# Performance work log

Measured on AMD Instinct MI355X. Metric: run time of the kernel, lower is better.

Reference implementation:

```python
import jax, jax.numpy as jnp
import numpy as np

W_GRID, H_GRID = 5, 5
N_NODES = W_GRID * H_GRID  # 25
N_NEI = 8
N_CLS = 10
BN_EPS = 1e-5


def _neighbors(i, w, h):
    """Replicates Brain.neighbors ordering exactly; pads missing slots with -1
    (the torch code pads with p1 == zeros at the END of the list)."""
    size = w * h
    n = []
    if i - w >= 0:
        n.append(i - w)
    if i % w != 0:
        n.append(i - 1)
    if (i + 1) % w != 0:
        n.append(i + 1)
    if i + w < size:
        n.append(i + w)
    if i - w - 1 >= 0 and i % w != 0:
        n.append(i - w - 1)
    if i - w + 1 >= 0 and (i + 1) % w != 0:
        n.append(i - w + 1)
    if i + w - 1 < size and i % w != 0:
        n.append(i + w - 1)
    if i + w + 1 < size and (i + 1) % w != 0:
        n.append(i + w + 1)
    while len(n) < N_NEI:
        n.append(-1)
    return n

NEI = np.array([_neighbors(i, W_GRID, H_GRID) for i in range(N_NODES)], dtype=np.int32)  # [25, 8]
NEI_CLIP = np.maximum(NEI, 0)
NEI_MASK = (NEI >= 0)


def conv_bn_relu(x, W, b, g, be, m, v):
    # Conv2d(k=3, s=1, p=1) + eval-mode BatchNorm2d + ReLU, NCHW layout
    y = jax.lax.conv_general_dilated(
        x, W, window_strides=(1, 1), padding=[(1, 1), (1, 1)],
        dimension_numbers=("NCHW", "OIHW", "NCHW"))
    y = y + b[None, :, None, None]
    scale = g / jnp.sqrt(v + BN_EPS)
    y = (y - m[None, :, None, None]) * scale[None, :, None, None] + be[None, :, None, None]
    return jax.nn.relu(y)


def maxpool3s2p1(x):
    # MaxPool2d(kernel=3, stride=2, padding=1)
    return jax.lax.reduce_window(
        x, -jnp.inf, jax.lax.max,
        window_dimensions=(1, 1, 3, 3), window_strides=(1, 1, 2, 2),
        padding=[(0, 0), (0, 0), (1, 1), (1, 1)])


def per_node_mlp(inp, Wa, ba, Wb, bb):
    # inp: [25, B, 336]; distinct Linear(336,600)-Tanh-Linear(600,10)-Softmax per node
    h = jnp.tanh(jnp.einsum("nbi,nih->nbh", inp, Wa) + ba[:, None, :])
    logits = jnp.einsum("nbh,nhc->nbc", h, Wb) + bb[:, None, :]
    return jax.nn.softmax(logits, axis=-1)  # [25, B, 10]


def setup_inputs() -> dict:
    key = jax.random.key(0)
    ks = iter(jax.random.split(key, 64))
    B, C = 8192, 3
    d = {"x": jax.random.normal(next(ks), (B, C, 20, 20), jnp.float32)}
    chans = [(C, 64), (64, 128), (128, 256), (256, 256)]
    for li, (ci, co) in enumerate(chans, start=1):
        d[f"W{li}"] = jax.random.normal(next(ks), (co, ci, 3, 3), jnp.float32) * 0.05
        d[f"b{li}"] = jax.random.normal(next(ks), (co,), jnp.float32) * 0.05
        d[f"g{li}"] = jax.random.uniform(next(ks), (co,), jnp.float32, 0.5, 1.5)
        d[f"be{li}"] = jax.random.normal(next(ks), (co,), jnp.float32) * 0.1
        d[f"m{li}"] = jax.random.normal(next(ks), (co,), jnp.float32) * 0.1
        d[f"v{li}"] = jax.random.uniform(next(ks), (co,), jnp.float32, 0.5, 1.5)
    d["Wa"] = jax.random.normal(next(ks), (N_NODES, 336, 600), jnp.float32) * 0.05
    d["ba"] = jax.random.normal(next(ks), (N_NODES, 600), jnp.float32) * 0.05
    d["Wb"] = jax.random.normal(next(ks), (N_NODES, 600, N_CLS), jnp.float32) * 0.05
    d["bb"] = jax.random.normal(next(ks), (N_NODES, N_CLS), jnp.float32) * 0.05
    return d


def reference(x, W1, b1, g1, be1, m1, v1, W2, b2, g2, be2, m2, v2,
              W3, b3, g3, be3, m3, v3, W4, b4, g4, be4, m4, v4,
              Wa, ba, Wb, bb):
    c = conv_bn_relu(x, W1, b1, g1, be1, m1, v1)
    c = maxpool3s2p1(c)                      # [B, 64, 10, 10]
    c = conv_bn_relu(c, W2, b2, g2, be2, m2, v2)
    c = maxpool3s2p1(c)                      # [B, 128, 5, 5]
    c = conv_bn_relu(c, W3, b3, g3, be3, m3, v3)
    c = conv_bn_relu(c, W4, b4, g4, be4, m4, v4)  # [B, 256, 5, 5]
    B = x.shape[0]
    feats = c.reshape(B, 256, N_NODES).transpose(2, 0, 1)  # [25, B, 256]
    # Stage 1: neighbor slots are all zeros (p1..p8 = zeros)
    zeros80 = jnp.zeros((N_NODES, B, N_NEI * N_CLS), x.dtype)
    preds = per_node_mlp(jnp.concatenate([zeros80, feats], axis=-1), Wa, ba, Wb, bb)  # [25, B, 10]
    # Stage 2: gather up to 8 neighbor predictions (ordered), pad missing with zeros
    nb = preds[jnp.asarray(NEI_CLIP)]                          # [25, 8, B, 10]
    nb = jnp.where(jnp.asarray(NEI_MASK)[:, :, None, None], nb, 0.0)
    nb = nb.transpose(0, 2, 1, 3).reshape(N_NODES, B, N_NEI * N_CLS)  # [25, B, 80]
    second = per_node_mlp(jnp.concatenate([nb, feats], axis=-1), Wa, ba, Wb, bb)  # [25, B, 10]
    mean_predictions = second.mean(axis=0)  # [B, 10]
    return mean_predictions, second
```

## Files before the change

### kernel.cpp

```cpp
#include <hip/hip_runtime.h>

typedef unsigned short u16;
typedef unsigned int u32;

typedef __attribute__((ext_vector_type(8))) __bf16 bf16x8;
typedef __attribute__((ext_vector_type(4))) float f32x4;

__device__ __forceinline__ float bf2f(u16 u) {
    u32 t = ((u32)u) << 16;
    float f;
    __builtin_memcpy(&f, &t, 4);
    return f;
}
__device__ __forceinline__ u16 f2bf(float f) {
    u32 u;
    __builtin_memcpy(&u, &f, 4);
    u32 r = (u + 0x7fffu + ((u >> 16) & 1u)) >> 16;
    return (u16)r;
}
__device__ __forceinline__ float tanh_fast(float x) {
    float xc = fminf(fmaxf(x, -15.f), 15.f);
    float e = __expf(2.f * xc);
    return (e - 1.f) * __builtin_amdgcn_rcpf(e + 1.f);
}

__device__ __forceinline__ void gld16(const u16* g, u16* l) {
    __builtin_amdgcn_global_load_lds(
        (const __attribute__((address_space(1))) u32*)(uintptr_t)g,
        (__attribute__((address_space(3))) u32*)(u32)(uintptr_t)l,
        16, 0, 0);
}


template <int EPI, int NT>
__global__ __launch_bounds__(256, 3) void gemm_bt(
    const u16* __restrict__ A, const u16* __restrict__ W, u16* __restrict__ O,
    const float* __restrict__ epiA, const float* __restrict__ epiB,
    int Kin, int N, int T, int Himg, int Wimg,
    int ldA, int ldW, int ldO,
    long long Az, long long Wz, long long Oz, int epiZ,
    int Bc, int bshift)
{
    constexpr int NJ = NT / 32;
    __shared__ __align__(16) u16 lsA[2][128 * 32];
    __shared__ __align__(16) u16 lsW[2][NT * 32];

    const int tid = threadIdx.x;
    const int z = blockIdx.z;
    A += (long long)z * Az;
    W += (long long)z * Wz;
    O += (long long)z * Oz;
    epiB += (long long)z * epiZ;

    const int m0 = blockIdx.x * 128;
    const int n0 = blockIdx.y * NT;
    const int s = m0 >> bshift;
    const int b0 = m0 & (Bc - 1);
    const int hh0 = s / Wimg, ww0 = s % Wimg;

    const int wave = tid >> 6;
    const int lane = tid & 63;
    const int mbase = (wave >> 1) * 64;
    const int nbase = (wave & 1) * (NT / 2);
    const int ln = lane & 15, qd = lane >> 4;

    const int srow = lane >> 2;
    const int sc = (((lane & 3) - ((srow >> 1) & 3)) & 3) * 8;
    const int csel = ((qd + (ln >> 1)) & 3) * 8;

    const int rowA = wave * 32 + srow;
    const int rowW = (NT == 128) ? (wave * 32 + srow) : (wave * 16 + srow);
    const int offA0 = rowA * ldA + sc;
    const int offA1 = offA0 + 16 * ldA;
    const int offW0 = rowW * ldW + sc;
    const int offW1 = offW0 + 16 * ldW;
    u16* const lA0 = &lsA[0][0] + wave * 1024;
    u16* const lW0 = (NT == 128) ? (&lsW[0][0] + wave * 1024) : (&lsW[0][0] + wave * 512);
    constexpr int LPAR_A = 128 * 32;
    constexpr int LPAR_W = NT * 32;

    auto tapvalid = [&](int t) -> bool {
        if (T != 9) return true;
        const int hh = hh0 + t / 3 - 1, ww = ww0 + t % 3 - 1;
        return hh >= 0 && hh < Himg && ww >= 0 && ww < Wimg;
    };
    auto tapA = [&](int t) -> const u16* {
        int sp = s;
        if (T == 9) sp = (hh0 + t / 3 - 1) * Wimg + (ww0 + t % 3 - 1);
        return A + (long long)(sp * Bc + b0) * ldA;
    };

    int t0 = 0;
    while (!tapvalid(t0)) ++t0;
    int nvalid = 0;
    for (int t = 0; t < T; ++t) nvalid += tapvalid(t) ? 1 : 0;
    const int KS = Kin >> 5;
    const int S = nvalid * KS;

    const u16* Ab = tapA(t0);
    const u16* Wb = W + ((long long)t0 * N + n0) * ldW;

    gld16(Ab + offA0, lA0);
    gld16(Ab + offA1, lA0 + 512);
    gld16(Wb + offW0, lW0);
    if (NT == 128) gld16(Wb + offW1, lW0 + 512);

    int ntap = t0, nkk = 0;

    f32x4 acc[4][NJ];
#pragma unroll
    for (int i = 0; i < 4; ++i)
#pragma unroll
        for (int j = 0; j < NJ; ++j)
            acc[i][j] = (f32x4){0.f, 0.f, 0.f, 0.f};

    for (int st = 0; st < S; ++st) {
        __syncthreads();
        if (st + 1 < S) {
            nkk += 32;
            if (nkk == Kin) {
                nkk = 0;
                do { ++ntap; } while (!tapvalid(ntap));
                Ab = tapA(ntap);
                Wb = W + ((long long)ntap * N + n0) * ldW;
            }
            const int pp = (st + 1) & 1;
            gld16(Ab + offA0 + nkk, lA0 + pp * LPAR_A);
            gld16(Ab + offA1 + nkk, lA0 + pp * LPAR_A + 512);
            gld16(Wb + offW0 + nkk, lW0 + pp * LPAR_W);
            if (NT == 128) gld16(Wb + offW1 + nkk, lW0 + pp * LPAR_W + 512);
        }
        const int cp = st & 1;
        bf16x8 af[4], bfr[NJ];
#pragma unroll
        for (int f = 0; f < 4; ++f)
            af[f] = *(const bf16x8*)&lsA[cp][(mbase + f * 16 + ln) * 32 + csel];
#pragma unroll
        for (int f = 0; f < NJ; ++f)
            bfr[f] = *(const bf16x8*)&lsW[cp][(nbase + f * 16 + ln) * 32 + csel];
#pragma unroll
        for (int i = 0; i < 4; ++i)
#pragma unroll
            for (int j = 0; j < NJ; ++j)
                acc[i][j] = __builtin_amdgcn_mfma_f32_16x16x32_bf16(
                    af[i], bfr[j], acc[i][j], 0, 0, 0);
    }

#pragma unroll
    for (int j = 0; j < NJ; ++j) {
        const int n = n0 + nbase + j * 16 + ln;
        const float sh = epiB[n];
        float sc2 = 1.f;
        if (EPI == 0) sc2 = epiA[n];
#pragma unroll
        for (int i = 0; i < 4; ++i) {
            const int mrow = mbase + i * 16 + qd * 4;
#pragma unroll
            for (int rr = 0; rr < 4; ++rr) {
                float v = acc[i][j][rr];
                if (EPI == 0) v = fmaxf(v * sc2 + sh, 0.f);
                else          v = tanh_fast(v + sh);
                O[(long long)(m0 + mrow + rr) * ldO + n] = f2bf(v);
            }
        }
    }
}

template <int STAGE>
__global__ __launch_bounds__(256, 2) void mlp_head(
    const u16* __restrict__ A, const u16* __restrict__ W,
    const float* __restrict__ bap, const u16* __restrict__ Wbp,
    const float* __restrict__ bbp,
    u16* __restrict__ preds, float* __restrict__ dout,
    int Kin, int Bc, int gbase)
{
    __shared__ __align__(16) u16 lsA[2][128 * 32];
    __shared__ __align__(16) u16 lsW[2][128 * 32];
    __shared__ __align__(16) u16 lsH[128 * 132];

    const int tid = threadIdx.x;
    const int z = blockIdx.z;
    A += (long long)z * Bc * Kin;
    W += (long long)z * 640 * 352;
    const float* bz = bap + z * 640;

    const int m0 = blockIdx.x * 128;
    const int wave = tid >> 6;
    const int lane = tid & 63;
    const int mbase = (wave >> 1) * 64;
    const int nbase = (wave & 1) * 64;
    const int ln = lane & 15, qd = lane >> 4;
    const int srow = lane >> 2;
    const int sc = (((lane & 3) - ((srow >> 1) & 3)) & 3) * 8;
    const int csel = ((qd + (ln >> 1)) & 3) * 8;

    const int rowS = wave * 32 + srow;
    const int offA0 = rowS * Kin + sc;
    const int offA1 = offA0 + 16 * Kin;
    const int offW0 = rowS * 352 + sc;
    const int offW1 = offW0 + 16 * 352;
    u16* const lA0 = &lsA[0][0] + wave * 1024;
    u16* const lW0 = &lsW[0][0] + wave * 1024;

    const int KS = Kin >> 5;
    const int Stot = 5 * KS;

    const u16* Ab = A + (long long)m0 * Kin;
    const u16* Wb = W;
    int pnt = 0, pnkk = 0;

    gld16(Ab + offA0, lA0);
    gld16(Ab + offA1, lA0 + 512);
    gld16(Wb + offW0, lW0);
    gld16(Wb + offW1, lW0 + 512);

    f32x4 acc[4][4];
#pragma unroll
    for (int i = 0; i < 4; ++i)
#pragma unroll
        for (int j = 0; j < 4; ++j)
            acc[i][j] = (f32x4){0.f, 0.f, 0.f, 0.f};
    f32x4 acc_lg[2];
    acc_lg[0] = (f32x4){0.f, 0.f, 0.f, 0.f};
    acc_lg[1] = (f32x4){0.f, 0.f, 0.f, 0.f};

    int g = 0;
    for (int nt = 0; nt < 5; ++nt) {
        for (int st = 0; st < KS; ++st, ++g) {
            __syncthreads();
            if (g + 1 < Stot) {
                pnkk += 32;
                if (pnkk == Kin) {
                    pnkk = 0;
                    ++pnt;
                    Wb = W + (long long)pnt * 128 * 352;
                }
                const int pp = (g + 1) & 1;
                gld16(Ab + offA0 + pnkk, lA0 + pp * (128 * 32));
                gld16(Ab + offA1 + pnkk, lA0 + pp * (128 * 32) + 512);
                gld16(Wb + offW0 + pnkk, lW0 + pp * (128 * 32));
                gld16(Wb + offW1 + pnkk, lW0 + pp * (128 * 32) + 512);
            }
            const int cp = g & 1;
            bf16x8 af[4], bfr[4];
#pragma unroll
            for (int f = 0; f < 4; ++f)
                af[f] = *(const bf16x8*)&lsA[cp][(mbase + f * 16 + ln) * 32 + csel];
#pragma unroll
            for (int f = 0; f < 4; ++f)
                bfr[f] = *(const bf16x8*)&lsW[cp][(nbase + f * 16 + ln) * 32 + csel];
#pragma unroll
            for (int i = 0; i < 4; ++i)
#pragma unroll
                for (int j = 0; j < 4; ++j)
                    acc[i][j] = __builtin_amdgcn_mfma_f32_16x16x32_bf16(
                        af[i], bfr[j], acc[i][j], 0, 0, 0);
        }

#pragma unroll
        for (int j = 0; j < 4; ++j) {
            const int hc = nbase + j * 16 + ln;
            const float sh = bz[nt * 128 + hc];
#pragma unroll
            for (int i = 0; i < 4; ++i) {
                const int br = mbase + i * 16 + qd * 4;
#pragma unroll
                for (int rr = 0; rr < 4; ++rr)
                    lsH[(br + rr) * 132 + hc] = f2bf(tanh_fast(acc[i][j][rr] + sh));
                acc[i][j] = (f32x4){0.f, 0.f, 0.f, 0.f};
            }
        }
        bf16x8 bfrg[4];
#pragma unroll
        for (int ks = 0; ks < 4; ++ks)
            bfrg[ks] = *(const bf16x8*)&Wbp[((long long)z * 16 + ln) * 640 +
                                            nt * 128 + ks * 32 + qd * 8];
        __syncthreads();

#pragma unroll
        for (int ks = 0; ks < 4; ++ks) {
#pragma unroll
            for (int i = 0; i < 2; ++i) {
                const int base = (wave * 32 + i * 16 + ln) * 132 + ks * 32 + qd * 8;
                const uint2 u0 = *(const uint2*)&lsH[base];
                const uint2 u1 = *(const uint2*)&lsH[base + 4];
                u32 w4[4] = {u0.x, u0.y, u1.x, u1.y};
                bf16x8 a8;
                __builtin_memcpy(&a8, w4, 16);
                acc_lg[i] = __builtin_amdgcn_mfma_f32_16x16x32_bf16(
                    a8, bfrg[ks], acc_lg[i], 0, 0, 0);
            }
        }
    }

    const float bias = bbp[z * 16 + ln];
#pragma unroll
    for (int i = 0; i < 2; ++i) {
#pragma unroll
        for (int rr = 0; rr < 4; ++rr) {
            const float v = acc_lg[i][rr] + bias;
            float mx = v;
#pragma unroll
            for (int mk = 1; mk < 16; mk <<= 1)
                mx = fmaxf(mx, __shfl_xor(mx, mk));
            const float e = __expf(v - mx);
            float ssum = e;
#pragma unroll
            for (int mk = 1; mk < 16; mk <<= 1)
                ssum += __shfl_xor(ssum, mk);
            const float p = e / ssum;
            const int row = m0 + wave * 32 + i * 16 + qd * 4 + rr;
            if (ln < 10) {
                if (STAGE == 1)
                    preds[((long long)z * Bc + row) * 10 + ln] = f2bf(p);
                else
                    dout[81920 + ((long long)z * 8192 + gbase + row) * 10 + ln] = p;
            }
        }
    }
}

__global__ __launch_bounds__(256) void conv1pool(
    const u16* __restrict__ xcol, const u16* __restrict__ W1t, u16* __restrict__ p1,
    const float* __restrict__ epiA, const float* __restrict__ epiB, int Bc)
{
    const int tid = threadIdx.x;
    const int wave = tid >> 6;
    const int lane = tid & 63;
    const int ln = lane & 15, qd = lane >> 4;

    const int b0 = blockIdx.x * 128;
    const int so = blockIdx.y;
    const int ho = so / 10, wo = so % 10;

    const int mbase = (wave >> 1) * 64;
    const int nbase = (wave & 1) * 32;

    bf16x8 bfr[2];
#pragma unroll
    for (int j = 0; j < 2; ++j)
        bfr[j] = *(const bf16x8*)&W1t[(nbase + j * 16 + ln) * 32 + qd * 8];

    float sc2[2], sh[2];
#pragma unroll
    for (int j = 0; j < 2; ++j) {
        const int n = nbase + j * 16 + ln;
        sc2[j] = epiA[n];
        sh[j] = epiB[n];
    }

    f32x4 best[4][2];
#pragma unroll
    for (int i = 0; i < 4; ++i)
#pragma unroll
        for (int j = 0; j < 2; ++j)
            best[i][j] = (f32x4){0.f, 0.f, 0.f, 0.f};

#pragma unroll
    for (int st = 0; st < 9; ++st) {
        int hh = 2 * ho - 1 + st / 3;
        int ww = 2 * wo - 1 + st % 3;
        hh = hh < 0 ? 0 : (hh > 19 ? 19 : hh);
        ww = ww < 0 ? 0 : (ww > 19 ? 19 : ww);
        const u16* Ab = xcol + (long long)((hh * 20 + ww) * Bc + b0) * 32;

        bf16x8 af[4];
#pragma unroll
        for (int f = 0; f < 4; ++f)
            af[f] = *(const bf16x8*)&Ab[(mbase + f * 16 + ln) * 32 + qd * 8];

#pragma unroll
        for (int i = 0; i < 4; ++i)
#pragma unroll
            for (int j = 0; j < 2; ++j) {
                f32x4 acc = (f32x4){0.f, 0.f, 0.f, 0.f};
                acc = __builtin_amdgcn_mfma_f32_16x16x32_bf16(af[i], bfr[j], acc, 0, 0, 0);
#pragma unroll
                for (int rr = 0; rr < 4; ++rr) {
                    const float v = fmaxf(acc[rr] * sc2[j] + sh[j], 0.f);
                    best[i][j][rr] = fmaxf(best[i][j][rr], v);
                }
            }
    }

#pragma unroll
    for (int j = 0; j < 2; ++j) {
        const int n = nbase + j * 16 + ln;
#pragma unroll
        for (int i = 0; i < 4; ++i) {
            const int mrow = mbase + i * 16 + qd * 4;
#pragma unroll
            for (int rr = 0; rr < 4; ++rr)
                p1[(long long)(so * Bc + b0 + mrow + rr) * 64 + n] = f2bf(best[i][j][rr]);
        }
    }
}

__global__ __launch_bounds__(256) void transpose_x(
    const float* __restrict__ x, u16* __restrict__ xt, int Bc, int bshift)
{
    const int t = blockIdx.x * 256 + threadIdx.x;
    if (t >= 400 * Bc) return;
    const int s = t >> bshift;
    const int b = t & (Bc - 1);
    const u32 c0 = f2bf(x[((long long)b * 3 + 0) * 400 + s]);
    const u32 c1 = f2bf(x[((long long)b * 3 + 1) * 400 + s]);
    const u32 c2 = f2bf(x[((long long)b * 3 + 2) * 400 + s]);
    uint2 st;
    st.x = c0 | (c1 << 16);
    st.y = c2;
    *(uint2*)(xt + ((long long)s * Bc + b) * 4) = st;
}

__global__ __launch_bounds__(256) void im2col1(
    const u16* __restrict__ xt, u16* __restrict__ xcol, int Bc, int bshift)
{
    const int t = blockIdx.x * 256 + threadIdx.x;
    if (t >= 400 * Bc) return;
    const int s = t >> bshift;
    const int b = t & (Bc - 1);
    const int hh = s / 20, ww = s % 20;

    u32 p0, q0, p1, q1, p2, q2, p3, q3, p4, q4, p5, q5, p6, q6, p7, q7, p8, q8;
#define LOADTAP(T, P, Q)                                                      \
    {                                                                         \
        const int ih = hh + (T) / 3 - 1, iw = ww + (T) % 3 - 1;               \
        P = 0u; Q = 0u;                                                       \
        if (ih >= 0 && ih < 20 && iw >= 0 && iw < 20) {                       \
            const uint2 v = *(const uint2*)(xt +                              \
                ((long long)(ih * 20 + iw) * Bc + b) * 4);                    \
            P = v.x; Q = v.y;                                                 \
        }                                                                     \
    }
    LOADTAP(0, p0, q0) LOADTAP(1, p1, q1) LOADTAP(2, p2, q2)
    LOADTAP(3, p3, q3) LOADTAP(4, p4, q4) LOADTAP(5, p5, q5)
    LOADTAP(6, p6, q6) LOADTAP(7, p7, q7) LOADTAP(8, p8, q8)
#undef LOADTAP

    u16* o = xcol + (long long)t * 32;
    uint4 w;
    w.x = p0;                w.y = q0 | (p1 << 16);
    w.z = (p1 >> 16) | (q1 << 16);
    w.w = p2;
    *(uint4*)(o + 0) = w;
    w.x = q2 | (p3 << 16);   w.y = (p3 >> 16) | (q3 << 16);
    w.z = p4;                w.w = q4 | (p5 << 16);
    *(uint4*)(o + 8) = w;
    w.x = (p5 >> 16) | (q5 << 16);
    w.y = p6;                w.z = q6 | (p7 << 16);
    w.w = (p7 >> 16) | (q7 << 16);
    *(uint4*)(o + 16) = w;
    w.x = p8;                w.y = q8;
    w.z = 0u;                w.w = 0u;
    *(uint4*)(o + 24) = w;
}

template <int CH>
__global__ __launch_bounds__(256) void pool_k(
    const u16* __restrict__ src, u16* __restrict__ dst, int Bc, int Hi, int Ho)
{
    constexpr int G = CH / 8;
    const int t = blockIdx.x * 256 + threadIdx.x;
    const int cc = t & (G - 1);
    const int b = t / G;
    if (b >= Bc) return;
    const int so = blockIdx.y;
    const int ho = so / Ho, wo = so % Ho;
    float best[8];
#pragma unroll
    for (int e = 0; e < 8; ++e) best[e] = 0.f;
    for (int ph = 0; ph < 3; ++ph) {
        const int hh = 2 * ho - 1 + ph;
        if (hh < 0 || hh >= Hi) continue;
        for (int pw = 0; pw < 3; ++pw) {
            const int ww = 2 * wo - 1 + pw;
            if (ww < 0 || ww >= Hi) continue;
            const uint4 u = *(const uint4*)(src + ((long long)(hh * Hi + ww) * Bc + b) * CH + cc * 8);
            const u32 uw[4] = {u.x, u.y, u.z, u.w};
#pragma unroll
            for (int e = 0; e < 4; ++e) {
                best[2 * e]     = fmaxf(best[2 * e],     bf2f((u16)(uw[e] & 0xffff)));
                best[2 * e + 1] = fmaxf(best[2 * e + 1], bf2f((u16)(uw[e] >> 16)));
            }
        }
    }
    u32 pk[4];
#pragma unroll
    for (int e = 0; e < 4; ++e)
        pk[e] = (u32)f2bf(best[2 * e]) | (((u32)f2bf(best[2 * e + 1])) << 16);
    uint4 st;
    st.x = pk[0]; st.y = pk[1]; st.z = pk[2]; st.w = pk[3];
    *(uint4*)(dst + ((long long)so * Bc + b) * CH + cc * 8) = st;
}

__device__ __forceinline__ void neighbors5x5(int i, int* nb) {
    const int w = 5, size = 25;
    int cnt = 0;
    if (i - w >= 0) nb[cnt++] = i - w;
    if (i % w != 0) nb[cnt++] = i - 1;
    if ((i + 1) % w != 0) nb[cnt++] = i + 1;
    if (i + w < size) nb[cnt++] = i + w;
    if (i - w - 1 >= 0 && i % w != 0) nb[cnt++] = i - w - 1;
    if (i - w + 1 >= 0 && (i + 1) % w != 0) nb[cnt++] = i - w + 1;
    if (i + w - 1 < size && i % w != 0) nb[cnt++] = i + w - 1;
    if (i + w + 1 < size && (i + 1) % w != 0) nb[cnt++] = i + w + 1;
    for (; cnt < 8; ++cnt) nb[cnt] = -1;
}

__global__ __launch_bounds__(256) void gather_nb(
    const u16* __restrict__ preds, const u16* __restrict__ feats, u16* __restrict__ A2,
    int Bc, int bshift)
{
    const int g = blockIdx.x * 256 + threadIdx.x;
    if (g >= 25 * Bc) return;
    const int n = g >> bshift;
    const int b = g & (Bc - 1);
    int nb[8];
    neighbors5x5(n, nb);
    u16* dst = A2 + (long long)g * 352;
#pragma unroll
    for (int j = 0; j < 8; ++j) {
        u32* d32 = (u32*)(dst + j * 10);
        if (nb[j] >= 0) {
            const u32* s32 = (const u32*)(preds + ((long long)nb[j] * Bc + b) * 10);
#pragma unroll
            for (int q = 0; q < 5; ++q) d32[q] = s32[q];
        } else {
#pragma unroll
            for (int q = 0; q < 5; ++q) d32[q] = 0u;
        }
    }
    const uint4* fs = (const uint4*)(feats + (long long)g * 256);
    uint4* fd = (uint4*)(dst + 80);
#pragma unroll
    for (int q = 0; q < 32; ++q) fd[q] = fs[q];
    uint4 z;
    z.x = 0u; z.y = 0u; z.z = 0u; z.w = 0u;
    *(uint4*)(dst + 336) = z;
    *(uint4*)(dst + 344) = z;
}

__global__ __launch_bounds__(256) void mean_k(float* __restrict__ dout)
{
    const int t = blockIdx.x * 256 + threadIdx.x;
    float s = 0.f;
#pragma unroll
    for (int n = 0; n < 25; ++n) s += dout[81920 + n * 81920 + t];
    dout[t] = s * 0.04f;
}

__global__ void prep_bn_all(
    const float* b1, const float* g1, const float* be1, const float* m1, const float* v1,
    const float* b2, const float* g2, const float* be2, const float* m2, const float* v2,
    const float* b3, const float* g3, const float* be3, const float* m3, const float* v3,
    const float* b4, const float* g4, const float* be4, const float* m4, const float* v4,
    float* bnA, float* bnB)
{
    const int t = blockIdx.x * 256 + threadIdx.x;
    if (t >= 704) return;
    const float *bp, *gp, *bep, *mp, *vp;
    int idx;
    if (t < 64)       { bp=b1; gp=g1; bep=be1; mp=m1; vp=v1; idx=t; }
    else if (t < 192) { bp=b2; gp=g2; bep=be2; mp=m2; vp=v2; idx=t-64; }
    else if (t < 448) { bp=b3; gp=g3; bep=be3; mp=m3; vp=v3; idx=t-192; }
    else              { bp=b4; gp=g4; bep=be4; mp=m4; vp=v4; idx=t-448; }
    const float A = gp[idx] * rsqrtf(vp[idx] + 1e-5f);
    bnA[t] = A;
    bnB[t] = (bp[idx] - mp[idx]) * A + bep[idx];
}

__global__ void prep_w1col(const float* __restrict__ W1, u16* __restrict__ W1t)
{
    const int t = blockIdx.x * 256 + threadIdx.x;
    if (t >= 64 * 32) return;
    const int n = t >> 5, k = t & 31;
    u16 v = 0;
    if (k < 27) {
        const int tap = k / 3, ci = k % 3;
        v = f2bf(W1[n * 27 + ci * 9 + tap]);
    }
    W1t[t] = v;
}

__global__ void prep_convw(const float* __restrict__ W, u16* __restrict__ Wt, int Co, int Ci)
{
    const int t = blockIdx.x * 256 + threadIdx.x;
    const int tot = 9 * Co * Ci;
    if (t >= tot) return;
    const int sh = t / (Co * Ci);
    const int rem = t % (Co * Ci);
    const int co = rem / Ci, ci = rem % Ci;
    Wt[t] = f2bf(W[(long long)(co * Ci + ci) * 9 + sh]);
}

__global__ void prep_wat(const float* __restrict__ Wa, u16* __restrict__ Wat)
{
    const int t = blockIdx.x * 256 + threadIdx.x;
    if (t >= 25 * 640 * 352) return;
    const int n = t / (640 * 352);
    const int rem = t % (640 * 352);
    const int hcol = rem / 352;
    const int k = rem % 352;
    float v = 0.f;
    if (hcol < 600 && k < 336) v = Wa[((long long)n * 336 + k) * 600 + hcol];
    Wat[t] = f2bf(v);
}

__global__ void prep_ba(const float* __restrict__ ba, float* __restrict__ bap)
{
    const int t = blockIdx.x * 256 + threadIdx.x;
    if (t >= 25 * 640) return;
    const int n = t / 640, hcol = t % 640;
    bap[t] = (hcol < 600) ? ba[n * 600 + hcol] : 0.f;
}

__global__ void prep_wbt(const float* __restrict__ Wb, const float* __restrict__ bb,
                         u16* __restrict__ Wbp, float* __restrict__ bbp)
{
    const int t = blockIdx.x * 256 + threadIdx.x;
    if (t < 25 * 16 * 640) {
        const int n = t / (16 * 640);
        const int rem = t % (16 * 640);
        const int c = rem / 640, k = rem % 640;
        u16 v = 0;
        if (c < 10 && k < 600) v = f2bf(Wb[((long long)n * 600 + k) * 10 + c]);
        Wbp[t] = v;
    }
    if (t < 25 * 16) {
        const int n = t >> 4, c = t & 15;
        bbp[t] = (c < 10) ? bb[n * 10 + c] : -1e30f;
    }
}

extern "C" void kernel_launch(void* const* d_in, const int* in_sizes, int n_in,
                              void* d_out, int out_size, void* d_ws, size_t ws_size,
                              hipStream_t stream)
{
    (void)in_sizes; (void)n_in; (void)out_size;

    const float* x  = (const float*)d_in[0];
    const float* W1 = (const float*)d_in[1];
    const float* b1 = (const float*)d_in[2];
    const float* g1 = (const float*)d_in[3];
    const float* be1= (const float*)d_in[4];
    const float* m1 = (const float*)d_in[5];
    const float* v1 = (const float*)d_in[6];
    const float* W2 = (const float*)d_in[7];
    const float* b2 = (const float*)d_in[8];
    const float* g2 = (const float*)d_in[9];
    const float* be2= (const float*)d_in[10];
    const float* m2 = (const float*)d_in[11];
    const float* v2 = (const float*)d_in[12];
    const float* W3 = (const float*)d_in[13];
    const float* b3 = (const float*)d_in[14];
    const float* g3 = (const float*)d_in[15];
    const float* be3= (const float*)d_in[16];
    const float* m3 = (const float*)d_in[17];
    const float* v3 = (const float*)d_in[18];
    const float* W4 = (const float*)d_in[19];
    const float* b4 = (const float*)d_in[20];
    const float* g4 = (const float*)d_in[21];
    const float* be4= (const float*)d_in[22];
    const float* m4 = (const float*)d_in[23];
    const float* v4 = (const float*)d_in[24];
    const float* Wa = (const float*)d_in[25];
    const float* ba = (const float*)d_in[26];
    const float* Wb = (const float*)d_in[27];
    const float* bb = (const float*)d_in[28];
    float* dout = (float*)d_out;

    auto al = [](long long v) { return (v + 255LL) & ~255LL; };
    const long long fixedB = al(4096) + al(147456) + al(589824) + al(1179648) +
                             al(11264000) + al(64000) + al(2816) + al(2816) +
                             al(512000) + al(1600);
    int Bc = 256;
    for (int cand = 8192; cand >= 256; cand >>= 1) {
        long long need = fixedB + al(44032LL * cand);
        if (need <= (long long)ws_size) { Bc = cand; break; }
    }
    const int bshift = __builtin_ctz((unsigned)Bc);
    const int C = 8192 / Bc;

    char* wsp = (char*)d_ws;
    long long off = 0;
    auto alloc = [&](long long bytes) { long long o = off; off += al(bytes); return o; };
    u16* W1t  = (u16*)(wsp + alloc(4096));
    u16* Wt2  = (u16*)(wsp + alloc(147456));
    u16* Wt3  = (u16*)(wsp + alloc(589824));
    u16* Wt4  = (u16*)(wsp + alloc(1179648));
    u16* Wat  = (u16*)(wsp + alloc(11264000));
    float* bap = (float*)(wsp + alloc(64000));
    float* bnA = (float*)(wsp + alloc(2816));
    float* bnB = (float*)(wsp + alloc(2816));
    u16* Wbp  = (u16*)(wsp + alloc(512000));
    float* bbp = (float*)(wsp + alloc(1600));
    char* ch = wsp + alloc(44032LL * Bc);
    u16* xt   = (u16*)(ch + 0LL     * Bc);
    u16* xcol = (u16*)(ch + 3200LL  * Bc);
    u16* p1   = (u16*)(ch + 28800LL * Bc);
    u16* a2   = (u16*)(ch + 0LL     * Bc);
    u16* p2   = (u16*)(ch + 25600LL * Bc);
    u16* a3   = (u16*)(ch + 0LL     * Bc);
    u16* a4   = (u16*)(ch + 12800LL * Bc);
    u16* preds= (u16*)(ch + 25600LL * Bc);
    u16* A2   = (u16*)(ch + 26112LL * Bc);

    prep_bn_all<<<dim3(3), 256, 0, stream>>>(b1,g1,be1,m1,v1, b2,g2,be2,m2,v2,
                                             b3,g3,be3,m3,v3, b4,g4,be4,m4,v4, bnA, bnB);
    prep_w1col<<<dim3(8), 256, 0, stream>>>(W1, W1t);
    prep_convw<<<dim3(288),  256, 0, stream>>>(W2, Wt2, 128, 64);
    prep_convw<<<dim3(1152), 256, 0, stream>>>(W3, Wt3, 256, 128);
    prep_convw<<<dim3(2304), 256, 0, stream>>>(W4, Wt4, 256, 256);
    prep_wat<<<dim3(22000), 256, 0, stream>>>(Wa, Wat);
    prep_ba<<<dim3(63), 256, 0, stream>>>(ba, bap);
    prep_wbt<<<dim3(1000), 256, 0, stream>>>(Wb, bb, Wbp, bbp);

    for (int c = 0; c < C; ++c) {
        const float* xc = x + (long long)c * Bc * 1200;

        transpose_x<<<dim3(400 * Bc / 256), 256, 0, stream>>>(xc, xt, Bc, bshift);
        im2col1<<<dim3(400 * Bc / 256), 256, 0, stream>>>(xt, xcol, Bc, bshift);
        conv1pool<<<dim3(Bc / 128, 100), 256, 0, stream>>>(xcol, W1t, p1, bnA, bnB, Bc);

        gemm_bt<0,128><<<dim3(100 * Bc / 128, 1), 256, 0, stream>>>(p1, Wt2, a2, bnA + 64, bnB + 64,
            64, 128, 9, 10, 10, 64, 64, 128, 0LL, 0LL, 0LL, 0, Bc, bshift);
        pool_k<128><<<dim3(Bc * 16 / 256, 25), 256, 0, stream>>>(a2, p2, Bc, 10, 5);

        gemm_bt<0,128><<<dim3(25 * Bc / 128, 2), 256, 0, stream>>>(p2, Wt3, a3, bnA + 192, bnB + 192,
            128, 256, 9, 5, 5, 128, 128, 256, 0LL, 0LL, 0LL, 0, Bc, bshift);
        gemm_bt<0,128><<<dim3(25 * Bc / 128, 2), 256, 0, stream>>>(a3, Wt4, a4, bnA + 448, bnB + 448,
            256, 256, 9, 5, 5, 256, 256, 256, 0LL, 0LL, 0LL, 0, Bc, bshift);

        mlp_head<1><<<dim3(Bc / 128, 1, 25), 256, 0, stream>>>(
            a4, Wat + 80, bap, Wbp, bbp, preds, nullptr, 256, Bc, 0);

        gather_nb<<<dim3(25 * Bc / 256, 1), 256, 0, stream>>>(preds, a4, A2, Bc, bshift);
        mlp_head<2><<<dim3(Bc / 128, 1, 25), 256, 0, stream>>>(
            A2, Wat, bap, Wbp, bbp, nullptr, dout, 352, Bc, c * Bc);
    }

    mean_k<<<dim3(320), 256, 0, stream>>>(dout);
}
```

Before: 1.398 ms.

## Add XCD-aware block swizzle and halve MLP head hidden LDS tile for occupancy

Adds an XCD-aware remapping of workgroup indices in the conv GEMM, conv1pool and MLP head kernels, so that neighbouring tiles land on the same XCD and share its L2. In the MLP head, the hidden-activation LDS staging buffer is split into two 64-column halves, each written and consumed in turn. This roughly halves that buffer so three blocks can be resident per CU (launch bounds raised to 3). The cost is extra barriers per hidden tile, and half the waves sit idle during each tanh write phase.

```diff
diff --git a/kernel.cpp b/kernel.cpp
--- a/kernel.cpp
+++ b/kernel.cpp
@@ -29,6 +29,12 @@
         (const __attribute__((address_space(1))) u32*)(uintptr_t)g,
         (__attribute__((address_space(3))) u32*)(u32)(uintptr_t)l,
         16, 0, 0);
+}
+
+__device__ __forceinline__ int xcd_swz(int orig, int nwg) {
+    const int xcd = orig & 7, base = orig >> 3;
+    const int q = nwg >> 3, r = nwg & 7;
+    return (xcd < r ? xcd * (q + 1) : r * (q + 1) + (xcd - r) * q) + base;
 }
 
 
@@ -52,7 +58,7 @@
     O += (long long)z * Oz;
     epiB += (long long)z * epiZ;
 
-    const int m0 = blockIdx.x * 128;
+    const int m0 = xcd_swz(blockIdx.x, gridDim.x) * 128;
     const int n0 = blockIdx.y * NT;
     const int s = m0 >> bshift;
     const int b0 = m0 & (Bc - 1);
@@ -167,7 +173,7 @@
 }
 
 template <int STAGE>
-__global__ __launch_bounds__(256, 2) void mlp_head(
+__global__ __launch_bounds__(256, 3) void mlp_head(
     const u16* __restrict__ A, const u16* __restrict__ W,
     const float* __restrict__ bap, const u16* __restrict__ Wbp,
     const float* __restrict__ bbp,
@@ -176,19 +182,23 @@
 {
     __shared__ __align__(16) u16 lsA[2][128 * 32];
     __shared__ __align__(16) u16 lsW[2][128 * 32];
-    __shared__ __align__(16) u16 lsH[128 * 132];
+    __shared__ __align__(16) u16 lsH[128 * 68];
 
     const int tid = threadIdx.x;
-    const int z = blockIdx.z;
+    const int nwg = gridDim.x * 25;
+    const int lin = xcd_swz(blockIdx.z * gridDim.x + blockIdx.x, nwg);
+    const int z = lin / gridDim.x;
+    const int m0 = (lin % gridDim.x) * 128;
+
     A += (long long)z * Bc * Kin;
     W += (long long)z * 640 * 352;
     const float* bz = bap + z * 640;
 
-    const int m0 = blockIdx.x * 128;
     const int wave = tid >> 6;
     const int lane = tid & 63;
     const int mbase = (wave >> 1) * 64;
     const int nbase = (wave & 1) * 64;
+    const int wsel = wave & 1;
     const int ln = lane & 15, qd = lane >> 4;
     const int srow = lane >> 2;
     const int sc = (((lane & 3) - ((srow >> 1) & 3)) & 3) * 8;
@@ -258,39 +268,50 @@
         }
 
 #pragma unroll
-        for (int j = 0; j < 4; ++j) {
-            const int hc = nbase + j * 16 + ln;
-            const float sh = bz[nt * 128 + hc];
-#pragma unroll
-            for (int i = 0; i < 4; ++i) {
-                const int br = mbase + i * 16 + qd * 4;
-#pragma unroll
-                for (int rr = 0; rr < 4; ++rr)
-                    lsH[(br + rr) * 132 + hc] = f2bf(tanh_fast(acc[i][j][rr] + sh));
-                acc[i][j] = (f32x4){0.f, 0.f, 0.f, 0.f};
+        for (int cc = 0; cc < 2; ++cc) {
+            if (cc) __syncthreads();
+            if (wsel == cc) {
+#pragma unroll
+                for (int j = 0; j < 4; ++j) {
+                    const int hcl = j * 16 + ln;
+                    const float sh = bz[nt * 128 + cc * 64 + hcl];
+#pragma unroll
+                    for (int i = 0; i < 4; ++i) {
+                        const int br = mbase + i * 16 + qd * 4;
+#pragma unroll
+                        for (int rr = 0; rr < 4; ++rr)
+                            lsH[(br + rr) * 68 + hcl] =
+                                f2bf(tanh_fast(acc[i][j][rr] + sh));
+                    }
+                }
+            }
+            bf16x8 bfrg[2];
+#pragma unroll
+            for (int ks = 0; ks < 2; ++ks)
+                bfrg[ks] = *(const bf16x8*)&Wbp[((long long)z * 16 + ln) * 640 +
+                                                nt * 128 + cc * 64 + ks * 32 + qd * 8];
+            __syncthreads();
+
+#pragma unroll
+            for (int ks = 0; ks < 2; ++ks) {
+#pragma unroll
+                for (int i = 0; i < 2; ++i) {
+                    const int base = (wave * 32 + i * 16 + ln) * 68 + ks * 32 + qd * 8;
+                    const uint2 u0 = *(const uint2*)&lsH[base];
+                    const uint2 u1 = *(const uint2*)&lsH[base + 4];
+                    u32 w4[4] = {u0.x, u0.y, u1.x, u1.y};
+                    bf16x8 a8;
+                    __builtin_memcpy(&a8, w4, 16);
+                    acc_lg[i] = __builtin_amdgcn_mfma_f32_16x16x32_bf16(
+                        a8, bfrg[ks], acc_lg[i], 0, 0, 0);
+                }
             }
         }
-        bf16x8 bfrg[4];
-#pragma unroll
-        for (int ks = 0; ks < 4; ++ks)
-            bfrg[ks] = *(const bf16x8*)&Wbp[((long long)z * 16 + ln) * 640 +
-                                            nt * 128 + ks * 32 + qd * 8];
-        __syncthreads();
-
-#pragma unroll
-        for (int ks = 0; ks < 4; ++ks) {
-#pragma unroll
-            for (int i = 0; i < 2; ++i) {
-                const int base = (wave * 32 + i * 16 + ln) * 132 + ks * 32 + qd * 8;
-                const uint2 u0 = *(const uint2*)&lsH[base];
-                const uint2 u1 = *(const uint2*)&lsH[base + 4];
-                u32 w4[4] = {u0.x, u0.y, u1.x, u1.y};
-                bf16x8 a8;
-                __builtin_memcpy(&a8, w4, 16);
-                acc_lg[i] = __builtin_amdgcn_mfma_f32_16x16x32_bf16(
-                    a8, bfrg[ks], acc_lg[i], 0, 0, 0);
-            }
-        }
+#pragma unroll
+        for (int i = 0; i < 4; ++i)
+#pragma unroll
+            for (int j = 0; j < 4; ++j)
+                acc[i][j] = (f32x4){0.f, 0.f, 0.f, 0.f};
     }
 
     const float bias = bbp[z * 16 + ln];
@@ -329,8 +350,10 @@
     const int lane = tid & 63;
     const int ln = lane & 15, qd = lane >> 4;
 
-    const int b0 = blockIdx.x * 128;
-    const int so = blockIdx.y;
+    const int nwg = gridDim.x * gridDim.y;
+    const int lin = xcd_swz(blockIdx.y * gridDim.x + blockIdx.x, nwg);
+    const int b0 = (lin % gridDim.x) * 128;
+    const int so = lin / gridDim.x;
     const int ho = so / 10, wo = so % 10;
 
     const int mbase = (wave >> 1) * 64;
```

Result: slower. 1.592 ms (+13.8%).
